# Kernel tuning notes

Hardware: AMD Instinct MI355X
Metric: run time of the kernel (lower is better)

## Reference

```python
import jax, jax.numpy as jnp
import numpy as np

PREF_DIM = 2
PREF_EMB = 64
HIDDEN = 512
NUM_CHUNKS = 105
CHUNK_EMB = 64
NUM_WS = 11
W_DIM = 20000


def setup_inputs() -> dict:
    key = jax.random.key(0)
    ks = jax.random.split(key, 12)
    in_dim = PREF_EMB + CHUNK_EMB
    inp = {
        "preference": jax.random.uniform(ks[0], (PREF_DIM,), dtype=jnp.float32),
        "pref_emb": 0.1 * jax.random.normal(ks[1], (PREF_DIM, PREF_EMB), dtype=jnp.float32),
        "chunk_emb": 0.1 * jax.random.normal(ks[2], (NUM_CHUNKS, CHUNK_EMB), dtype=jnp.float32),
        "W1": jax.random.normal(ks[3], (HIDDEN, in_dim), dtype=jnp.float32) / np.sqrt(in_dim),
        "b1": jnp.zeros((HIDDEN,), dtype=jnp.float32),
        "W2": jax.random.normal(ks[4], (HIDDEN, HIDDEN), dtype=jnp.float32) / np.sqrt(HIDDEN),
        "b2": jnp.zeros((HIDDEN,), dtype=jnp.float32),
        "W3": jax.random.normal(ks[5], (HIDDEN, HIDDEN), dtype=jnp.float32) / np.sqrt(HIDDEN),
        "b3": jnp.zeros((HIDDEN,), dtype=jnp.float32),
        "ws": 0.1 * jax.random.normal(ks[6], (NUM_WS, W_DIM, HIDDEN), dtype=jnp.float32),
    }
    return inp


def reference(preference, pref_emb, chunk_emb, W1, b1, W2, b2, W3, b3, ws):
    # pref_embedding = sum_i preference[i] * pref_emb[i]  -> [PREF_EMB]
    pref_embedding = preference @ pref_emb
    # Batch all chunks: concat(pref_embedding, chunk_emb[c]) -> [C, PREF_EMB+CHUNK_EMB]
    C = chunk_emb.shape[0]
    x = jnp.concatenate(
        [jnp.broadcast_to(pref_embedding, (C, pref_embedding.shape[0])), chunk_emb],
        axis=1,
    )
    # 3-layer MLP (Linear/ReLU/Linear/ReLU/Linear)
    h = jax.nn.relu(x @ W1.T + b1)
    h = jax.nn.relu(h @ W2.T + b2)
    rep = h @ W3.T + b3  # [C, HIDDEN]
    # Per chunk, concat over ws of F.linear(rep, w): [C, NUM_WS, W_DIM]
    out = jnp.einsum("ch,kwh->ckw", rep, ws)
    # Flat weight vector (original then reshapes contiguous slices into a dict;
    # that slicing is a pure view op on this vector)
    return out.reshape(-1)
```

## Files before the change

kernel.cpp:

```cpp
#include <hip/hip_runtime.h>


typedef __bf16 bf16x8 __attribute__((ext_vector_type(8)));
typedef float f32x4 __attribute__((ext_vector_type(4)));

#define NUM_CHUNKS 105
#define HIDDEN 512
#define N_COLS 220000
#define REP_FRAG_BYTES 114688

__global__ void mlp_kernel(const float* __restrict__ pref,
                           const float* __restrict__ pref_emb,
                           const float* __restrict__ chunk_emb,
                           const float* __restrict__ W1, const float* __restrict__ b1,
                           const float* __restrict__ W2, const float* __restrict__ b2,
                           const float* __restrict__ W3, const float* __restrict__ b3,
                           __bf16* __restrict__ repf) {
  __shared__ float x[128];
  __shared__ float h1[512];
  __shared__ float h2[512];
  const int tid = threadIdx.x;
  const int c = blockIdx.x;

  if (tid < 64) {
    x[tid] = pref[0] * pref_emb[tid] + pref[1] * pref_emb[64 + tid];
  } else if (tid < 128) {
    x[tid] = chunk_emb[c * 64 + (tid - 64)];
  }
  __syncthreads();

  for (int jj = tid; jj < 512; jj += 256) {
    float s = b1[jj];
    const f32x4* wr = (const f32x4*)(W1 + jj * 128);
#pragma unroll
    for (int i = 0; i < 32; ++i) {
      f32x4 w = wr[i];
      s += w[0] * x[i * 4 + 0] + w[1] * x[i * 4 + 1] +
           w[2] * x[i * 4 + 2] + w[3] * x[i * 4 + 3];
    }
    h1[jj] = fmaxf(s, 0.f);
  }
  __syncthreads();

  for (int jj = tid; jj < 512; jj += 256) {
    float s = b2[jj];
    const f32x4* wr = (const f32x4*)(W2 + jj * 512);
#pragma unroll 8
    for (int i = 0; i < 128; ++i) {
      f32x4 w = wr[i];
      s += w[0] * h1[i * 4 + 0] + w[1] * h1[i * 4 + 1] +
           w[2] * h1[i * 4 + 2] + w[3] * h1[i * 4 + 3];
    }
    h2[jj] = fmaxf(s, 0.f);
  }
  __syncthreads();

  const int t = c >> 4, mmc = c & 15;
  for (int jj = tid; jj < 512; jj += 256) {
    float s = b3[jj];
    const f32x4* wr = (const f32x4*)(W3 + jj * 512);
#pragma unroll 8
    for (int i = 0; i < 128; ++i) {
      f32x4 w = wr[i];
      s += w[0] * h2[i * 4 + 0] + w[1] * h2[i * 4 + 1] +
           w[2] * h2[i * 4 + 2] + w[3] * h2[i * 4 + 3];
    }
    const int ss = jj >> 5, qq = (jj >> 3) & 3, j = jj & 7;
    const long idx = (((long)(ss * 7 + t) * 4 + qq) * 16 + mmc) * 8 + j;
    repf[idx] = (__bf16)s;
  }
}

__global__ void gemm_ws(const float* __restrict__ ws,
                        const bf16x8* __restrict__ repf,
                        float* __restrict__ out) {
  const int lane = threadIdx.x;
  const int q = lane >> 4;
  const int mm = lane & 15;
  const long cb = (long)blockIdx.x * 32;
  const long col0 = cb + mm;
  const long col1 = col0 + 16;

  const f32x4* w0 = (const f32x4*)(ws + col0 * 512) + q * 2;
  const f32x4* w1 = (const f32x4*)(ws + col1 * 512) + q * 2;

  f32x4 acc0[7], acc1[7];
#pragma unroll
  for (int t = 0; t < 7; ++t) {
    acc0[t] = (f32x4){0.f, 0.f, 0.f, 0.f};
    acc1[t] = (f32x4){0.f, 0.f, 0.f, 0.f};
  }

#pragma unroll 2
  for (int s = 0; s < 16; ++s) {
    f32x4 x0 = __builtin_nontemporal_load(w0 + s * 8);
    f32x4 x1 = __builtin_nontemporal_load(w0 + s * 8 + 1);
    f32x4 y0 = __builtin_nontemporal_load(w1 + s * 8);
    f32x4 y1 = __builtin_nontemporal_load(w1 + s * 8 + 1);
    bf16x8 b0, b1;
#pragma unroll
    for (int j = 0; j < 4; ++j) {
      b0[j] = (__bf16)x0[j];
      b0[4 + j] = (__bf16)x1[j];
      b1[j] = (__bf16)y0[j];
      b1[4 + j] = (__bf16)y1[j];
    }
    const bf16x8* ap = repf + s * 448 + lane;
#pragma unroll
    for (int t = 0; t < 7; ++t) {
      bf16x8 a = ap[t * 64];
      acc0[t] = __builtin_amdgcn_mfma_f32_16x16x32_bf16(a, b0, acc0[t], 0, 0, 0);
      acc1[t] = __builtin_amdgcn_mfma_f32_16x16x32_bf16(a, b1, acc1[t], 0, 0, 0);
    }
  }

#pragma unroll
  for (int t = 0; t < 7; ++t) {
    const int mbase = t * 16 + q * 4;
#pragma unroll
    for (int r = 0; r < 4; ++r) {
      const int m = mbase + r;
      if (m < NUM_CHUNKS) {
        __builtin_nontemporal_store(acc0[t][r], out + (long)m * N_COLS + col0);
        __builtin_nontemporal_store(acc1[t][r], out + (long)m * N_COLS + col1);
      }
    }
  }
}

extern "C" void kernel_launch(void* const* d_in, const int* in_sizes, int n_in,
                              void* d_out, int out_size, void* d_ws, size_t ws_size,
                              hipStream_t stream) {
  const float* pref      = (const float*)d_in[0];
  const float* pref_emb  = (const float*)d_in[1];
  const float* chunk_emb = (const float*)d_in[2];
  const float* W1 = (const float*)d_in[3];
  const float* b1 = (const float*)d_in[4];
  const float* W2 = (const float*)d_in[5];
  const float* b2 = (const float*)d_in[6];
  const float* W3 = (const float*)d_in[7];
  const float* b3 = (const float*)d_in[8];
  const float* ws = (const float*)d_in[9];
  float* out = (float*)d_out;
  __bf16* repf = (__bf16*)d_ws;

  hipMemsetAsync(d_ws, 0, REP_FRAG_BYTES, stream);
  mlp_kernel<<<NUM_CHUNKS, 256, 0, stream>>>(pref, pref_emb, chunk_emb,
                                             W1, b1, W2, b2, W3, b3, repf);
  gemm_ws<<<N_COLS / 32, 64, 0, stream>>>(ws, (const bf16x8*)d_ws, out);
}
```

Measured before the change: 731.3 us.

## Prefetch ws slices into registers, use 5-wave blocks, drop workspace memset

The GEMM kernel now launches 320-thread blocks where each wave handles its own 32-column tile. It software-prefetches the next k-slice of ws into registers while doing the current MFMAs, to hide global load latency. The memset of the rep fragment buffer is removed, relying on the fact that the uninitialized padding rows only affect output rows that are never stored. The MLP dot products use four independent accumulators to shorten the dependency chains. The register prefetch raises VGPR pressure in exchange.

```diff
diff --git a/kernel.cpp b/kernel.cpp
--- a/kernel.cpp
+++ b/kernel.cpp
@@ -5,9 +5,7 @@
 typedef float f32x4 __attribute__((ext_vector_type(4)));
 
 #define NUM_CHUNKS 105
-#define HIDDEN 512
 #define N_COLS 220000
-#define REP_FRAG_BYTES 114688
 
 __global__ void mlp_kernel(const float* __restrict__ pref,
                            const float* __restrict__ pref_emb,
@@ -30,54 +28,63 @@
   __syncthreads();
 
   for (int jj = tid; jj < 512; jj += 256) {
-    float s = b1[jj];
     const f32x4* wr = (const f32x4*)(W1 + jj * 128);
+    float s0 = 0.f, s1 = 0.f, s2 = 0.f, s3 = 0.f;
 #pragma unroll
     for (int i = 0; i < 32; ++i) {
       f32x4 w = wr[i];
-      s += w[0] * x[i * 4 + 0] + w[1] * x[i * 4 + 1] +
-           w[2] * x[i * 4 + 2] + w[3] * x[i * 4 + 3];
+      s0 += w[0] * x[i * 4 + 0];
+      s1 += w[1] * x[i * 4 + 1];
+      s2 += w[2] * x[i * 4 + 2];
+      s3 += w[3] * x[i * 4 + 3];
     }
-    h1[jj] = fmaxf(s, 0.f);
+    h1[jj] = fmaxf(b1[jj] + (s0 + s1) + (s2 + s3), 0.f);
   }
   __syncthreads();
 
   for (int jj = tid; jj < 512; jj += 256) {
-    float s = b2[jj];
     const f32x4* wr = (const f32x4*)(W2 + jj * 512);
+    float s0 = 0.f, s1 = 0.f, s2 = 0.f, s3 = 0.f;
 #pragma unroll 8
     for (int i = 0; i < 128; ++i) {
       f32x4 w = wr[i];
-      s += w[0] * h1[i * 4 + 0] + w[1] * h1[i * 4 + 1] +
-           w[2] * h1[i * 4 + 2] + w[3] * h1[i * 4 + 3];
+      s0 += w[0] * h1[i * 4 + 0];
+      s1 += w[1] * h1[i * 4 + 1];
+      s2 += w[2] * h1[i * 4 + 2];
+      s3 += w[3] * h1[i * 4 + 3];
     }
-    h2[jj] = fmaxf(s, 0.f);
+    h2[jj] = fmaxf(b2[jj] + (s0 + s1) + (s2 + s3), 0.f);
   }
   __syncthreads();
 
   const int t = c >> 4, mmc = c & 15;
   for (int jj = tid; jj < 512; jj += 256) {
-    float s = b3[jj];
     const f32x4* wr = (const f32x4*)(W3 + jj * 512);
+    float s0 = 0.f, s1 = 0.f, s2 = 0.f, s3 = 0.f;
 #pragma unroll 8
     for (int i = 0; i < 128; ++i) {
       f32x4 w = wr[i];
-      s += w[0] * h2[i * 4 + 0] + w[1] * h2[i * 4 + 1] +
-           w[2] * h2[i * 4 + 2] + w[3] * h2[i * 4 + 3];
+      s0 += w[0] * h2[i * 4 + 0];
+      s1 += w[1] * h2[i * 4 + 1];
+      s2 += w[2] * h2[i * 4 + 2];
+      s3 += w[3] * h2[i * 4 + 3];
     }
+    float s = b3[jj] + (s0 + s1) + (s2 + s3);
     const int ss = jj >> 5, qq = (jj >> 3) & 3, j = jj & 7;
-    const long idx = (((long)(ss * 7 + t) * 4 + qq) * 16 + mmc) * 8 + j;
+    const long idx = (long)(ss * 448 + t * 64 + qq * 16 + mmc) * 8 + j;
     repf[idx] = (__bf16)s;
   }
 }
 
-__global__ void gemm_ws(const float* __restrict__ ws,
-                        const bf16x8* __restrict__ repf,
-                        float* __restrict__ out) {
-  const int lane = threadIdx.x;
+__global__ __launch_bounds__(320) void gemm_ws(
+    const float* __restrict__ ws,
+    const bf16x8* __restrict__ repf,
+    float* __restrict__ out) {
+  const int lane = threadIdx.x & 63;
+  const int wv = threadIdx.x >> 6;
   const int q = lane >> 4;
   const int mm = lane & 15;
-  const long cb = (long)blockIdx.x * 32;
+  const long cb = (long)blockIdx.x * 160 + wv * 32;
   const long col0 = cb + mm;
   const long col1 = col0 + 16;
 
@@ -91,19 +98,27 @@
     acc1[t] = (f32x4){0.f, 0.f, 0.f, 0.f};
   }
 
-#pragma unroll 2
+  f32x4 c0 = __builtin_nontemporal_load(w0);
+  f32x4 c1 = __builtin_nontemporal_load(w0 + 1);
+  f32x4 c2 = __builtin_nontemporal_load(w1);
+  f32x4 c3 = __builtin_nontemporal_load(w1 + 1);
+
+#pragma unroll 4
   for (int s = 0; s < 16; ++s) {
-    f32x4 x0 = __builtin_nontemporal_load(w0 + s * 8);
-    f32x4 x1 = __builtin_nontemporal_load(w0 + s * 8 + 1);
-    f32x4 y0 = __builtin_nontemporal_load(w1 + s * 8);
-    f32x4 y1 = __builtin_nontemporal_load(w1 + s * 8 + 1);
+    f32x4 n0, n1, n2, n3;
+    if (s < 15) {
+      n0 = __builtin_nontemporal_load(w0 + (s + 1) * 8);
+      n1 = __builtin_nontemporal_load(w0 + (s + 1) * 8 + 1);
+      n2 = __builtin_nontemporal_load(w1 + (s + 1) * 8);
+      n3 = __builtin_nontemporal_load(w1 + (s + 1) * 8 + 1);
+    }
     bf16x8 b0, b1;
 #pragma unroll
     for (int j = 0; j < 4; ++j) {
-      b0[j] = (__bf16)x0[j];
-      b0[4 + j] = (__bf16)x1[j];
-      b1[j] = (__bf16)y0[j];
-      b1[4 + j] = (__bf16)y1[j];
+      b0[j] = (__bf16)c0[j];
+      b0[4 + j] = (__bf16)c1[j];
+      b1[j] = (__bf16)c2[j];
+      b1[4 + j] = (__bf16)c3[j];
     }
     const bf16x8* ap = repf + s * 448 + lane;
 #pragma unroll
@@ -112,6 +127,7 @@
       acc0[t] = __builtin_amdgcn_mfma_f32_16x16x32_bf16(a, b0, acc0[t], 0, 0, 0);
       acc1[t] = __builtin_amdgcn_mfma_f32_16x16x32_bf16(a, b1, acc1[t], 0, 0, 0);
     }
+    c0 = n0; c1 = n1; c2 = n2; c3 = n3;
   }
 
 #pragma unroll
@@ -144,8 +160,7 @@
   float* out = (float*)d_out;
   __bf16* repf = (__bf16*)d_ws;
 
-  hipMemsetAsync(d_ws, 0, REP_FRAG_BYTES, stream);
   mlp_kernel<<<NUM_CHUNKS, 256, 0, stream>>>(pref, pref_emb, chunk_emb,
                                              W1, b1, W2, b2, W3, b3, repf);
-  gemm_ws<<<N_COLS / 32, 64, 0, stream>>>(ws, (const bf16x8*)d_ws, out);
+  gemm_ws<<<N_COLS / 160, 320, 0, stream>>>(ws, (const bf16x8*)d_ws, out);
 }
```

Result: slower. 747.2 us (+2.2%).
